# Optimization experiments

Hardware: AMD Instinct MI355X
Metric: run time of the kernel (lower is better)

Reference implementation:

```python
import jax, jax.numpy as jnp
import numpy as np

NC = 10
STRIDES = (8, 16, 32)
REG_W = 5.0
GAMMA = 2.0
ALPHA = 0.25
CENTER_R = 2.5
TOPK = 10


def _bce_logits(x, t):
    # numerically stable BCEWithLogits, reduction='none'
    return jnp.clip(x, 0.0) - x * t + jnp.log1p(jnp.exp(-jnp.abs(x)))


def _decode(pred, stride):
    # pred: [B, 5+NC, H, W] -> [B, H*W, 5+NC] with xy=(p+grid)*s, wh=exp(p)*s
    B, C, H, W = pred.shape
    out = pred.reshape(B, C, H * W).transpose(0, 2, 1)
    yv, xv = jnp.meshgrid(jnp.arange(H), jnp.arange(W), indexing='ij')
    grid = jnp.stack([xv, yv], -1).reshape(H * W, 2).astype(pred.dtype)
    xy = (out[..., :2] + grid[None]) * stride
    wh = jnp.exp(out[..., 2:4]) * stride
    return jnp.concatenate([xy, wh, out[..., 4:]], -1), grid


def _pair_iou(gt, pr):
    # gt [G,4], pr [A,4] in xywh -> [G,A]
    a1 = gt[:, None, :2] - gt[:, None, 2:] * 0.5
    a2 = gt[:, None, :2] + gt[:, None, 2:] * 0.5
    b1 = pr[None, :, :2] - pr[None, :, 2:] * 0.5
    b2 = pr[None, :, :2] + pr[None, :, 2:] * 0.5
    wh = jnp.clip(jnp.minimum(a2, b2) - jnp.maximum(a1, b1), 0.0)
    inter = wh[..., 0] * wh[..., 1]
    return inter / (gt[:, None, 2] * gt[:, None, 3] + pr[None, :, 2] * pr[None, :, 3] - inter + 1e-8)


def _assign(gt_box, gt_cls, gt_valid, bbox, cls_logit, obj_logit, xc, yc, sa):
    # SimOTA dynamic-k assignment for one image (padded GT with validity mask).
    G = gt_box.shape[0]
    gx, gy, gw, gh = gt_box[:, 0], gt_box[:, 1], gt_box[:, 2], gt_box[:, 3]
    l = xc[None] - (gx - gw * 0.5)[:, None]
    r = (gx + gw * 0.5)[:, None] - xc[None]
    tt = yc[None] - (gy - gh * 0.5)[:, None]
    bb = (gy + gh * 0.5)[:, None] - yc[None]
    in_box = (jnp.minimum(jnp.minimum(l, r), jnp.minimum(tt, bb)) > 0.0) & gt_valid[:, None]
    rad = CENTER_R * sa[None]
    cl = xc[None] - gx[:, None] + rad
    cr = gx[:, None] + rad - xc[None]
    ct = yc[None] - gy[:, None] + rad
    cb = gy[:, None] + rad - yc[None]
    in_ctr = (jnp.minimum(jnp.minimum(cl, cr), jnp.minimum(ct, cb)) > 0.0) & gt_valid[:, None]
    fg = jnp.any(in_box | in_ctr, axis=0)                       # [A] candidate anchors
    in_both = in_box & in_ctr
    ious = _pair_iou(gt_box, bbox)                              # [G,A]
    ious_fg = jnp.where(fg[None] & gt_valid[:, None], ious, 0.0)
    p = jnp.sqrt(jax.nn.sigmoid(cls_logit)[None] * jax.nn.sigmoid(obj_logit)[None])  # [1,A,NC]
    tgt = jax.nn.one_hot(gt_cls, NC)[:, None]                   # [G,1,NC]
    cls_cost = -(tgt * jnp.log(p + 1e-12) + (1.0 - tgt) * jnp.log(1.0 - p + 1e-12)).sum(-1)
    cost = (cls_cost + 3.0 * (-jnp.log(ious + 1e-8))
            + 1e5 * (~in_both) + 1e6 * ((~fg)[None] | (~gt_valid)[:, None]))
    # dynamic k per GT from sum of top-10 IoUs
    topk_ious = jax.lax.top_k(ious_fg, TOPK)[0]
    dyn_k = jnp.clip(topk_ious.sum(-1).astype(jnp.int32), 1, None)  # [G]
    _, idx = jax.lax.top_k(-cost, TOPK)                             # lowest-cost anchors per GT
    sel = (jnp.arange(TOPK)[None, :] < dyn_k[:, None]) & gt_valid[:, None]
    matching = jnp.zeros(cost.shape, bool).at[jnp.arange(G)[:, None], idx].set(sel)
    n_match = matching.sum(0)
    best = jnp.argmin(cost, 0)
    # anchors matched to multiple GTs keep only the min-cost GT
    matching = jnp.where(n_match[None] > 1, jnp.arange(G)[:, None] == best[None], matching)
    fg_final = jnp.any(matching, 0)
    mg = jnp.argmax(matching, 0)
    miou = (matching * ious).sum(0)
    return fg_final, miou, gt_cls[mg], gt_box[mg]


def _forward(pred0, pred1, pred2, labels):
    decoded, grids, strd = [], [], []
    for p, s in zip((pred0, pred1, pred2), STRIDES):
        o, g = _decode(p, s)
        decoded.append(o)
        grids.append(g)
        strd.append(jnp.full((g.shape[0],), float(s), o.dtype))
    out = jnp.concatenate(decoded, 1)                # [B,A,5+NC]
    grid = jnp.concatenate(grids, 0)                 # [A,2]
    sa = jnp.concatenate(strd, 0)                    # [A]
    bbox, obj, cls = out[..., :4], out[..., 4:5], out[..., 5:]
    xc = (grid[:, 0] + 0.5) * sa
    yc = (grid[:, 1] + 0.5) * sa
    gt_valid = labels.sum(-1) > 0                    # [B,G]
    gt_cls = labels[..., 0].astype(jnp.int32)
    gt_box = labels[..., 1:5]
    sg = jax.lax.stop_gradient                       # assignment is @torch.no_grad
    fg, miou, mcls, rtgt = jax.vmap(_assign, in_axes=(0, 0, 0, 0, 0, 0, None, None, None))(
        gt_box, gt_cls, gt_valid, sg(bbox), sg(cls), sg(obj), xc, yc, sa)
    fgf = fg.astype(out.dtype)
    num_fg = jnp.maximum(fgf.sum(), 1.0)
    p1 = bbox[..., :2] - bbox[..., 2:] * 0.5
    p2 = bbox[..., :2] + bbox[..., 2:] * 0.5
    t1 = rtgt[..., :2] - rtgt[..., 2:] * 0.5
    t2 = rtgt[..., :2] + rtgt[..., 2:] * 0.5
    wh = jnp.clip(jnp.minimum(p2, t2) - jnp.maximum(p1, t1), 0.0)
    inter = wh[..., 0] * wh[..., 1]
    iou = inter / (bbox[..., 2] * bbox[..., 3] + rtgt[..., 2] * rtgt[..., 3] - inter + 1e-8)
    loss_iou = ((1.0 - iou ** 2) * fgf).sum() / num_fg
    # focal objectness loss (gamma=2.0, alpha=0.25)
    t = fgf[..., None]
    bce = _bce_logits(obj, t)
    pr = jax.nn.sigmoid(obj)
    pt = t * pr + (1.0 - t) * (1.0 - pr)
    loss_obj = (bce * (t * ALPHA + (1.0 - t) * (1.0 - ALPHA)) * (1.0 - pt) ** GAMMA).sum() / num_fg
    # classification loss (reporting only, nc>1)
    ctgt = jax.nn.one_hot(mcls, NC, dtype=out.dtype) * miou[..., None]
    loss_cls = (_bce_logits(cls, ctgt) * fgf[..., None]).sum() / num_fg
    total = REG_W * loss_iou + loss_obj
    return total, loss_iou, loss_obj, loss_cls


def setup_inputs() -> dict:
    key = jax.random.key(0)
    ks = jax.random.split(key, 7)
    B, G = 16, 60
    pred0 = jax.random.normal(ks[0], (B, 5 + NC, 160, 160), jnp.float32)
    pred1 = jax.random.normal(ks[1], (B, 5 + NC, 80, 80), jnp.float32)
    pred2 = jax.random.normal(ks[2], (B, 5 + NC, 40, 40), jnp.float32)
    cls = jax.random.randint(ks[3], (B, G, 1), 0, NC).astype(jnp.float32)
    cxy = jax.random.uniform(ks[4], (B, G, 2), minval=32.0, maxval=1248.0)
    wh = jax.random.uniform(ks[5], (B, G, 2), minval=16.0, maxval=256.0)
    ngt = jax.random.randint(ks[6], (B,), 5, G + 1)
    valid = (jnp.arange(G)[None, :] < ngt[:, None]).astype(jnp.float32)
    labels = jnp.concatenate([cls, cxy, wh], -1) * valid[..., None]
    return {"pred0": pred0, "pred1": pred1, "pred2": pred2, "labels": labels}


def reference(pred0, pred1, pred2, labels):
    return _forward(pred0, pred1, pred2, labels)
```

## Files before the change

### kernel.cpp

```cpp
#include <hip/hip_runtime.h>
#include <math.h>

#define NCLS 10
#define NB   16
#define NG   60
#define NA   33600
#define BA   (NB*NA)
#define NBLK_X 132
#define NBLK_LOSS (NBLK_X*NB)

__device__ double g_part[NBLK_LOSS][4];
__device__ int    g_fcount[NB];
__device__ int    g_nmatch[BA];
__device__ int    g_gsum[BA];
__device__ int    g_slot[BA];
__device__ float4 g_cbox [BA];
__device__ float4 g_cmeta[BA];
__device__ float  g_cD   [(size_t)NB*NCLS*NA];

__device__ __forceinline__ void anchor_geom(int a, int& H, int& W, float& s, int& h, int& w, int& lvl) {
  if (a < 25600)      { lvl = 0; H = 160; W = 160; s = 8.f;  h = a / 160;            w = a - h*160; }
  else if (a < 32000) { lvl = 1; H = 80;  W = 80;  s = 16.f; int r = a - 25600; h = r / 80;  w = r - h*80; }
  else                { lvl = 2; H = 40;  W = 40;  s = 32.f; int r = a - 32000; h = r / 40;  w = r - h*40; }
}

__device__ __forceinline__ unsigned int fkey(float f) {
  unsigned int b = __float_as_uint(f);
  return (b & 0x80000000u) ? ~b : (b | 0x80000000u);
}

__global__ __launch_bounds__(256) void decode_kernel(const float* __restrict__ p0,
                                                     const float* __restrict__ p1,
                                                     const float* __restrict__ p2,
                                                     const float* __restrict__ lb) {
  __shared__ float lab[NG*5];
  __shared__ int   glist[NG];
  __shared__ int   gln;
  __shared__ int   wbase[4];
  __shared__ int   bbase_s;
  int b = blockIdx.y, tid = threadIdx.x;
  for (int i = tid; i < NG*5; i += 256) lab[i] = lb[(size_t)b*NG*5 + i];
  if (tid == 0) gln = 0;
  __syncthreads();

  int a0 = blockIdx.x * 256;
  int H, W, h0, w0, lvl; float st;
  anchor_geom(a0, H, W, st, h0, w0, lvl);
  int aL = a0 + 255; if (aL >= NA) aL = NA - 1;
  int Hx, Wx, h1, w1, l1; float st1;
  anchor_geom(aL, Hx, Wx, st1, h1, w1, l1);
  float ylo = ((float)h0 + 0.5f) * st;
  float yhi = ((float)h1 + 0.5f) * st;
  float rad = 2.5f * st;

  if (tid < NG) {
    float s0 = lab[tid*5] + lab[tid*5+1] + lab[tid*5+2] + lab[tid*5+3] + lab[tid*5+4];
    if (s0 > 0.f) {
      float gy = lab[tid*5+2], gh = lab[tid*5+4];
      float m = fmaxf(gh * 0.5f, rad);
      if ((gy - m < yhi) && (gy + m > ylo)) {
        int p = atomicAdd(&gln, 1);
        glist[p] = tid;
      }
    }
  }
  __syncthreads();

  int n = gln;
  if (n == 0) return;

  int a = a0 + tid;
  bool valid = a < NA;
  int H2, W2, ht, wt, l2; float st2;
  anchor_geom(valid ? a : a0, H2, W2, st2, ht, wt, l2);
  float xc = ((float)wt + 0.5f) * st;
  float yc = ((float)ht + 0.5f) * st;

  int fg = 0;
  if (valid) {
    for (int q = 0; q < n; q++) {
      int g = glist[q];
      float gx = lab[g*5+1], gy = lab[g*5+2], gw = lab[g*5+3], gh = lab[g*5+4];
      float l  = xc - (gx - gw*0.5f);
      float r  = (gx + gw*0.5f) - xc;
      float t  = yc - (gy - gh*0.5f);
      float bo = (gy + gh*0.5f) - yc;
      float m1 = fminf(fminf(l, r), fminf(t, bo));
      float cl = xc - gx + rad, cr = gx + rad - xc, ct = yc - gy + rad, cb = gy + rad - yc;
      float m2 = fminf(fminf(cl, cr), fminf(ct, cb));
      if (m1 > 0.f || m2 > 0.f) { fg = 1; break; }
    }
  }

  unsigned long long m = __ballot(fg != 0);
  int lane = tid & 63, wv = tid >> 6;
  if (lane == 0) wbase[wv] = __popcll(m);
  __syncthreads();
  if (tid == 0) {
    int t = 0;
    #pragma unroll
    for (int k = 0; k < 4; k++) { int c = wbase[k]; wbase[k] = t; t += c; }
    bbase_s = t ? atomicAdd(&g_fcount[b], t) : 0;
  }
  __syncthreads();

  if (fg) {
    const float* pp = (lvl == 0) ? p0 : ((lvl == 1) ? p1 : p2);
    size_t cs = (size_t)H * W;
    size_t base = (size_t)b * 15 * cs + (size_t)ht * W + wt;

    float tx = pp[base], ty = pp[base+cs], tw = pp[base+2*cs], th = pp[base+3*cs], to = pp[base+4*cs];
    float4 boxv = make_float4((tx + (float)wt) * st, (ty + (float)ht) * st,
                              __expf(tw) * st, __expf(th) * st);

    float so = 1.f / (1.f + __expf(-to));
    float S = 0.f;
    float Dl[NCLS];
    #pragma unroll
    for (int c = 0; c < NCLS; c++) {
      float xl = pp[base + (size_t)(5 + c) * cs];
      float sc = 1.f / (1.f + __expf(-xl));
      float p  = sqrtf(sc * so);
      float L  = __logf(p + 1e-12f);
      float M  = __logf(1.f - p + 1e-12f);
      S += M;
      Dl[c] = L - M;
    }

    int j = bbase_s + wbase[wv] + (int)__popcll(m & ((1ULL << lane) - 1ULL));
    size_t cb = (size_t)b * NA + j;
    g_cbox[cb]  = boxv;
    g_cmeta[cb] = make_float4(xc, yc, S, __int_as_float(a));
    #pragma unroll
    for (int c = 0; c < NCLS; c++) g_cD[((size_t)b*NCLS + c)*NA + j] = Dl[c];
    g_slot[b * NA + a] = j;
  }
}

__global__ __launch_bounds__(256) void topk_kernel(const float* __restrict__ lb) {
  __shared__ unsigned long long keyarr[256];
  __shared__ unsigned long long kvl[4][10];
  __shared__ float              ioul[4][10];
  __shared__ int                wcnt[4];
  __shared__ int                sdynk;
  __shared__ int                st1cnt;

  int fid = blockIdx.x;
  int t8 = fid >> 3;
  int b  = ((fid & 7) << 1) + (t8 >= 60 ? 1 : 0);
  int g  = t8 - (t8 >= 60 ? 60 : 0);
  int tid = threadIdx.x, lane = tid & 63, wv = tid >> 6;

  const float* L = &lb[((size_t)b*NG + g)*5];
  float l0 = L[0], l1 = L[1], l2 = L[2], l3 = L[3], l4 = L[4];
  if (!(l0 + l1 + l2 + l3 + l4 > 0.f)) return;

  int   gc = (int)l0;
  float gx = l1, gy = l2, gw = l3, gh = l4;
  float a1x = gx - gw*0.5f, a1y = gy - gh*0.5f, a2x = gx + gw*0.5f, a2y = gy + gh*0.5f;
  float garea = gw * gh;
  int F = g_fcount[b];
  const float4* CB = &g_cbox [(size_t)b*NA];
  const float4* CM = &g_cmeta[(size_t)b*NA];
  const float*  CD = &g_cD[((size_t)b*NCLS + gc)*NA];

  unsigned long long t1key = ~0ULL;
  if (tid < 108) {
    int lv   = tid / 36;
    int cell = tid - lv*36;
    int dy   = cell / 6 - 2;
    int dx   = cell - (cell/6)*6 - 2;
    int   W  = (lv == 0) ? 160 : ((lv == 1) ? 80 : 40);
    float st = (lv == 0) ? 8.f : ((lv == 1) ? 16.f : 32.f);
    int   ab = (lv == 0) ? 0 : ((lv == 1) ? 25600 : 32000);
    int wc = (int)floorf(gx / st - 0.5f) + dx;
    int hc = (int)floorf(gy / st - 0.5f) + dy;
    if (wc >= 0 && wc < W && hc >= 0 && hc < W) {
      float xc = ((float)wc + 0.5f) * st;
      float yc = ((float)hc + 0.5f) * st;
      float rad = 2.5f * st;
      bool inb = fminf(fminf(xc - a1x, a2x - xc), fminf(yc - a1y, a2y - yc)) > 0.f;
      bool inc = fminf(fminf(xc - gx + rad, gx + rad - xc), fminf(yc - gy + rad, gy + rad - yc)) > 0.f;
      if (inb && inc) {
        int a = ab + hc * W + wc;
        int j = g_slot[b*NA + a];
        float4 B = CB[j];
        float Dv = CD[j];
        float S  = CM[j].z;
        float b1x = B.x - B.z*0.5f, b1y = B.y - B.w*0.5f;
        float b2x = B.x + B.z*0.5f, b2y = B.y + B.w*0.5f;
        float wx = fminf(a2x, b2x) - fmaxf(a1x, b1x); wx = wx > 0.f ? wx : 0.f;
        float wy = fminf(a2y, b2y) - fmaxf(a1y, b1y); wy = wy > 0.f ? wy : 0.f;
        float inter = wx * wy;
        float iou = inter / (garea + B.z*B.w - inter + 1e-8f);
        float cost = -(Dv + S) + 3.0f * (-__logf(iou + 1e-8f));
        t1key = ((unsigned long long)fkey(cost) << 32) | (unsigned int)a;
      }
    }
  }
  keyarr[tid] = t1key;
  {
    unsigned long long bal = __ballot(t1key != ~0ULL);
    if (lane == 0) wcnt[wv] = __popcll(bal);
  }

  float iv[10];
  #pragma unroll
  for (int k = 0; k < 10; k++) iv[k] = 0.f;
  #pragma unroll 2
  for (int j = tid; j < F; j += 256) {
    float4 B = CB[j];
    float b1x = B.x - B.z*0.5f, b1y = B.y - B.w*0.5f;
    float b2x = B.x + B.z*0.5f, b2y = B.y + B.w*0.5f;
    float wx = fminf(a2x, b2x) - fmaxf(a1x, b1x); wx = wx > 0.f ? wx : 0.f;
    float wy = fminf(a2y, b2y) - fmaxf(a1y, b1y); wy = wy > 0.f ? wy : 0.f;
    float inter = wx * wy;
    float iou = inter / (garea + B.z*B.w - inter + 1e-8f);
    if (iou > iv[9]) {
      iv[9] = iou;
      #pragma unroll
      for (int k = 9; k > 0; k--) {
        if (iv[k] > iv[k-1]) { float t = iv[k]; iv[k] = iv[k-1]; iv[k-1] = t; }
      }
    }
  }
  for (int k = 0; k < 10; k++) {
    float m = iv[0];
    #pragma unroll
    for (int d = 1; d < 64; d <<= 1) m = fmaxf(m, __shfl_xor(m, d));
    if (lane == 0) ioul[wv][k] = m;
    unsigned long long pm = __ballot(iv[0] == m);
    if (lane == __ffsll((unsigned long long)pm) - 1) {
      #pragma unroll
      for (int j2 = 0; j2 < 9; j2++) iv[j2] = iv[j2+1];
      iv[9] = 0.f;
    }
  }
  __syncthreads();

  if (tid == 0) {
    st1cnt = wcnt[0] + wcnt[1] + wcnt[2] + wcnt[3];
    int p_[4] = {0,0,0,0};
    float ss = 0.f;
    #pragma unroll 1
    for (int k = 0; k < 10; k++) {
      float best = ioul[0][p_[0]]; int bl = 0;
      #pragma unroll
      for (int l = 1; l < 4; l++) {
        float v = ioul[l][p_[l]];
        if (v > best) { best = v; bl = l; }
      }
      ss += best;
      if (p_[bl] < 9) p_[bl]++;
      else ioul[bl][9] = -INFINITY;
    }
    int dynk = (int)ss;
    if (dynk < 1)  dynk = 1;
    if (dynk > 10) dynk = 10;
    sdynk = dynk;
  }
  __syncthreads();
  int dynk  = sdynk;
  int t1cnt = st1cnt;

  if (t1cnt >= 10) {
    if (wv == 0) {
      unsigned long long q0 = keyarr[lane], q1 = keyarr[lane+64],
                         q2 = keyarr[lane+128], q3 = keyarr[lane+192];
      { unsigned long long t;
        if (q1 < q0) { t=q0; q0=q1; q1=t; }
        if (q3 < q2) { t=q2; q2=q3; q3=t; }
        if (q2 < q0) { t=q0; q0=q2; q2=t; }
        if (q3 < q1) { t=q1; q1=q3; q3=t; }
        if (q2 < q1) { t=q1; q1=q2; q2=t; } }
      for (int k = 0; k < dynk; k++) {
        unsigned long long m = q0;
        #pragma unroll
        for (int d = 1; d < 64; d <<= 1) {
          unsigned long long o = __shfl_xor(m, d);
          if (o < m) m = o;
        }
        if (m == ~0ULL) break;
        if (lane == 0) {
          int a = (int)(unsigned int)(m & 0xFFFFFFFFu);
          atomicAdd(&g_nmatch[b*NA + a], 1);
          atomicAdd(&g_gsum[b*NA + a], g);
        }
        if (q0 == m) { q0 = q1; q1 = q2; q2 = q3; q3 = ~0ULL; }
      }
    }
  } else {
    unsigned long long kv[10];
    #pragma unroll
    for (int k = 0; k < 10; k++) kv[k] = ~0ULL;
    for (int j = tid; j < F; j += 256) {
      float4 B = CB[j];
      float4 M = CM[j];
      float Dv = CD[j];
      int a = __float_as_int(M.w);
      float b1x = B.x - B.z*0.5f, b1y = B.y - B.w*0.5f;
      float b2x = B.x + B.z*0.5f, b2y = B.y + B.w*0.5f;
      float wx = fminf(a2x, b2x) - fmaxf(a1x, b1x); wx = wx > 0.f ? wx : 0.f;
      float wy = fminf(a2y, b2y) - fmaxf(a1y, b1y); wy = wy > 0.f ? wy : 0.f;
      float inter = wx * wy;
      float iou = inter / (garea + B.z*B.w - inter + 1e-8f);
      float xc = M.x, yc = M.y;
      float rad = (a < 25600) ? 20.f : ((a < 32000) ? 40.f : 80.f);
      bool inb = fminf(fminf(xc - a1x, a2x - xc), fminf(yc - a1y, a2y - yc)) > 0.f;
      bool inc = fminf(fminf(xc - gx + rad, gx + rad - xc), fminf(yc - gy + rad, gy + rad - yc)) > 0.f;
      float cost = -(Dv + M.z) + 3.0f * (-__logf(iou + 1e-8f));
      if (!(inb && inc)) cost += 100000.0f;
      unsigned long long key = ((unsigned long long)fkey(cost) << 32) | (unsigned int)a;
      if (key < kv[9]) {
        kv[9] = key;
        #pragma unroll
        for (int k = 9; k > 0; k--) {
          if (kv[k] < kv[k-1]) { unsigned long long t = kv[k]; kv[k] = kv[k-1]; kv[k-1] = t; }
        }
      }
    }
    for (int k = 0; k < 10; k++) {
      unsigned long long m = kv[0];
      #pragma unroll
      for (int d = 1; d < 64; d <<= 1) {
        unsigned long long o = __shfl_xor(m, d);
        if (o < m) m = o;
      }
      if (lane == 0) kvl[wv][k] = m;
      if (kv[0] == m) {
        #pragma unroll
        for (int j2 = 0; j2 < 9; j2++) kv[j2] = kv[j2+1];
        kv[9] = ~0ULL;
      }
    }
    __syncthreads();
    if (tid == 0) {
      int p_[4] = {0,0,0,0};
      #pragma unroll 1
      for (int k = 0; k < dynk; k++) {
        unsigned long long best = kvl[0][p_[0]]; int bl = 0;
        #pragma unroll
        for (int l = 1; l < 4; l++) {
          unsigned long long v = kvl[l][p_[l]];
          if (v < best) { best = v; bl = l; }
        }
        if (best == ~0ULL) break;
        int a = (int)(unsigned int)(best & 0xFFFFFFFFu);
        atomicAdd(&g_nmatch[b*NA + a], 1);
        atomicAdd(&g_gsum[b*NA + a], g);
        if (p_[bl] < 9) p_[bl]++;
        else kvl[bl][9] = ~0ULL;
      }
    }
  }
}

__global__ __launch_bounds__(256) void loss_kernel(const float* __restrict__ p0,
                                                   const float* __restrict__ p1,
                                                   const float* __restrict__ p2,
                                                   const float* __restrict__ lb) {
  __shared__ float  lab[NG*5];
  __shared__ int    lval[NG];
  __shared__ double red[256*4];
  int b = blockIdx.y, tid = threadIdx.x;
  for (int i = tid; i < NG*5; i += 256) lab[i] = lb[(size_t)b*NG*5 + i];
  __syncthreads();
  if (tid < NG) {
    float s = lab[tid*5] + lab[tid*5+1] + lab[tid*5+2] + lab[tid*5+3] + lab[tid*5+4];
    lval[tid] = (s > 0.f) ? 1 : 0;
  }
  __syncthreads();

  int a = blockIdx.x * 256 + tid;
  double t_nfg = 0.0, t_iou = 0.0, t_obj = 0.0, t_cls = 0.0;

  if (a < NA) {
    int idx = b * NA + a;
    int H, W, h, w, lvl; float st;
    anchor_geom(a, H, W, st, h, w, lvl);
    const float* pp = (lvl == 0) ? p0 : ((lvl == 1) ? p1 : p2);
    size_t cs = (size_t)H * W;
    size_t base = (size_t)b * 15 * cs + (size_t)h * W + w;

    float x  = pp[base + 4*cs];
    int   nm = g_nmatch[idx];
    float t  = (nm > 0) ? 1.f : 0.f;
    float bce = fmaxf(x, 0.f) - x * t + log1pf(expf(-fabsf(x)));
    float pr  = 1.f / (1.f + expf(-x));
    float pt  = (nm > 0) ? pr : (1.f - pr);
    float wf  = (nm > 0) ? 0.25f : 0.75f;
    float om  = 1.f - pt;
    t_obj = (double)(bce * wf * om * om);

    if (nm > 0) {
      t_nfg = 1.0;
      int mgsum = g_gsum[idx];
      g_nmatch[idx] = 0;
      g_gsum[idx]   = 0;
      int j = g_slot[idx];
      float4 B  = g_cbox [(size_t)b*NA + j];
      float4 Mt = g_cmeta[(size_t)b*NA + j];
      float pw = B.z, ph = B.w;
      float b1x = B.x - pw*0.5f, b1y = B.y - ph*0.5f, b2x = B.x + pw*0.5f, b2y = B.y + ph*0.5f;
      int mg;
      if (nm == 1) {
        mg = mgsum;
      } else {
        float xc = Mt.x, yc = Mt.y, S = Mt.z;
        float rad = 2.5f * st;
        const float* CDb = &g_cD[(size_t)b*NCLS*NA];
        float best = INFINITY; int bg = 0;
        for (int g = 0; g < NG; g++) {
          float gx = lab[g*5+1], gy = lab[g*5+2], gw = lab[g*5+3], gh = lab[g*5+4];
          int gcl = (int)lab[g*5];
          int v = lval[g];
          float a1x = gx - gw*0.5f, a1y = gy - gh*0.5f, a2x = gx + gw*0.5f, a2y = gy + gh*0.5f;
          float wx = fminf(a2x, b2x) - fmaxf(a1x, b1x); wx = wx > 0.f ? wx : 0.f;
          float wy = fminf(a2y, b2y) - fmaxf(a1y, b1y); wy = wy > 0.f ? wy : 0.f;
          float inter = wx * wy;
          float iou = inter / (gw*gh + pw*ph - inter + 1e-8f);
          float l = xc - a1x, r = a2x - xc, tt = yc - a1y, bo = a2y - yc;
          bool inb = (fminf(fminf(l, r), fminf(tt, bo)) > 0.f) && v;
          float cl = xc - gx + rad, cr = gx + rad - xc, ct = yc - gy + rad, cb = gy + rad - yc;
          bool inc = (fminf(fminf(cl, cr), fminf(ct, cb)) > 0.f) && v;
          float clsc = -(CDb[(size_t)gcl*NA + j] + S);
          float cost = clsc + 3.0f * (-__logf(iou + 1e-8f));
          if (!(inb && inc)) cost += 100000.0f;
          if (!v)            cost += 1000000.0f;
          if (cost < best) { best = cost; bg = g; }
        }
        mg = bg;
      }

      float gx = lab[mg*5+1], gy = lab[mg*5+2], gw = lab[mg*5+3], gh = lab[mg*5+4];
      int mcls = (int)lab[mg*5];
      float a1x = gx - gw*0.5f, a1y = gy - gh*0.5f, a2x = gx + gw*0.5f, a2y = gy + gh*0.5f;
      float wx = fminf(a2x, b2x) - fmaxf(a1x, b1x); wx = wx > 0.f ? wx : 0.f;
      float wy = fminf(a2y, b2y) - fmaxf(a1y, b1y); wy = wy > 0.f ? wy : 0.f;
      float inter = wx * wy;
      float miou = inter / (gw*gh + pw*ph - inter + 1e-8f);

      t_iou = (double)(1.f - miou * miou);

      float sc = 0.f;
      #pragma unroll
      for (int c = 0; c < NCLS; c++) {
        float xl = pp[base + (size_t)(5 + c) * cs];
        float ctg = (c == mcls) ? miou : 0.f;
        sc += fmaxf(xl, 0.f) - xl * ctg + log1pf(expf(-fabsf(xl)));
      }
      t_cls = (double)sc;
    }
  }

  red[tid] = t_nfg; red[256+tid] = t_iou; red[512+tid] = t_obj; red[768+tid] = t_cls;
  __syncthreads();
  for (int s = 128; s > 0; s >>= 1) {
    if (tid < s) {
      red[tid]     += red[tid+s];
      red[256+tid] += red[256+tid+s];
      red[512+tid] += red[512+tid+s];
      red[768+tid] += red[768+tid+s];
    }
    __syncthreads();
  }
  if (tid == 0) {
    int blk = b * NBLK_X + blockIdx.x;
    g_part[blk][0] = red[0];
    g_part[blk][1] = red[256];
    g_part[blk][2] = red[512];
    g_part[blk][3] = red[768];
  }
}

__global__ __launch_bounds__(256) void final_kernel(float* __restrict__ out) {
  __shared__ double red[256];
  int tid = threadIdx.x;
  int cat = tid & 3;
  double s = 0.0;
  for (int blk = tid >> 2; blk < NBLK_LOSS; blk += 64) s += g_part[blk][cat];
  red[tid] = s;
  __syncthreads();
  for (int st = 128; st >= 4; st >>= 1) {
    if (tid < st) red[tid] += red[tid + st];
    __syncthreads();
  }
  if (tid == 0) {
    double nfg = red[0];
    double num = (nfg < 1.0) ? 1.0 : nfg;
    float li = (float)(red[1] / num);
    float lo = (float)(red[2] / num);
    float lc = (float)(red[3] / num);
    out[0] = 5.0f * li + lo;
    out[1] = li;
    out[2] = lo;
    out[3] = lc;
  }
  if (tid < NB) g_fcount[tid] = 0;
}

extern "C" void kernel_launch(void* const* d_in, const int* in_sizes, int n_in,
                              void* d_out, int out_size, void* d_ws, size_t ws_size,
                              hipStream_t stream) {
  const float* p0 = (const float*)d_in[0];
  const float* p1 = (const float*)d_in[1];
  const float* p2 = (const float*)d_in[2];
  const float* lb = (const float*)d_in[3];
  float* out = (float*)d_out;

  hipLaunchKernelGGL(decode_kernel, dim3(NBLK_X, NB), dim3(256), 0, stream, p0, p1, p2, lb);
  hipLaunchKernelGGL(topk_kernel,   dim3(NB*NG), dim3(256), 0, stream, lb);
  hipLaunchKernelGGL(loss_kernel,   dim3(NBLK_X, NB), dim3(256), 0, stream, p0, p1, p2, lb);
  hipLaunchKernelGGL(final_kernel,  dim3(1), dim3(256), 0, stream, out);
}
```

Measured before the change: 189.3 us.

## Widen topk blocks to 512 threads, prefetch boxes, use shuffle reduction in loss

The top-k assignment kernel now launches 512 threads per GT (8 wavefronts) and merges per-wave top-10 lists across 8 waves. Its IoU scan software-prefetches the next candidate box. The stage-1 key array shrinks to 128 entries, which assumes the hidden code produces at most 128 in-box-and-center candidates. The loss kernel replaces a shared-memory tree reduction over 4 double arrays with wave shuffles plus a small cross-wave sum, removing many barriers.

```diff
diff --git a/kernel.cpp b/kernel.cpp
--- a/kernel.cpp
+++ b/kernel.cpp
@@ -8,6 +8,7 @@
 #define BA   (NB*NA)
 #define NBLK_X 132
 #define NBLK_LOSS (NBLK_X*NB)
+#define TKW  8
 
 __device__ double g_part[NBLK_LOSS][4];
 __device__ int    g_fcount[NB];
@@ -137,11 +138,11 @@
   }
 }
 
-__global__ __launch_bounds__(256) void topk_kernel(const float* __restrict__ lb) {
-  __shared__ unsigned long long keyarr[256];
-  __shared__ unsigned long long kvl[4][10];
-  __shared__ float              ioul[4][10];
-  __shared__ int                wcnt[4];
+__global__ __launch_bounds__(512) void topk_kernel(const float* __restrict__ lb) {
+  __shared__ unsigned long long keyarr[128];
+  __shared__ unsigned long long kvl[TKW][10];
+  __shared__ float              ioul[TKW][10];
+  __shared__ int                wcnt[2];
   __shared__ int                sdynk;
   __shared__ int                st1cnt;
 
@@ -198,8 +199,8 @@
       }
     }
   }
-  keyarr[tid] = t1key;
-  {
+  if (tid < 128) keyarr[tid] = t1key;
+  if (wv < 2) {
     unsigned long long bal = __ballot(t1key != ~0ULL);
     if (lane == 0) wcnt[wv] = __popcll(bal);
   }
@@ -207,21 +208,28 @@
   float iv[10];
   #pragma unroll
   for (int k = 0; k < 10; k++) iv[k] = 0.f;
-  #pragma unroll 2
-  for (int j = tid; j < F; j += 256) {
-    float4 B = CB[j];
-    float b1x = B.x - B.z*0.5f, b1y = B.y - B.w*0.5f;
-    float b2x = B.x + B.z*0.5f, b2y = B.y + B.w*0.5f;
-    float wx = fminf(a2x, b2x) - fmaxf(a1x, b1x); wx = wx > 0.f ? wx : 0.f;
-    float wy = fminf(a2y, b2y) - fmaxf(a1y, b1y); wy = wy > 0.f ? wy : 0.f;
-    float inter = wx * wy;
-    float iou = inter / (garea + B.z*B.w - inter + 1e-8f);
-    if (iou > iv[9]) {
-      iv[9] = iou;
-      #pragma unroll
-      for (int k = 9; k > 0; k--) {
-        if (iv[k] > iv[k-1]) { float t = iv[k]; iv[k] = iv[k-1]; iv[k-1] = t; }
-      }
+  {
+    int j = tid;
+    float4 Bc = make_float4(0.f, 0.f, 0.f, 0.f);
+    if (j < F) Bc = CB[j];
+    while (j < F) {
+      int jn = j + 512;
+      float4 Bn = make_float4(0.f, 0.f, 0.f, 0.f);
+      if (jn < F) Bn = CB[jn];
+      float b1x = Bc.x - Bc.z*0.5f, b1y = Bc.y - Bc.w*0.5f;
+      float b2x = Bc.x + Bc.z*0.5f, b2y = Bc.y + Bc.w*0.5f;
+      float wx = fminf(a2x, b2x) - fmaxf(a1x, b1x); wx = wx > 0.f ? wx : 0.f;
+      float wy = fminf(a2y, b2y) - fmaxf(a1y, b1y); wy = wy > 0.f ? wy : 0.f;
+      float inter = wx * wy;
+      float iou = inter / (garea + Bc.z*Bc.w - inter + 1e-8f);
+      if (iou > iv[9]) {
+        iv[9] = iou;
+        #pragma unroll
+        for (int k = 9; k > 0; k--) {
+          if (iv[k] > iv[k-1]) { float t = iv[k]; iv[k] = iv[k-1]; iv[k-1] = t; }
+        }
+      }
+      Bc = Bn; j = jn;
     }
   }
   for (int k = 0; k < 10; k++) {
@@ -239,14 +247,16 @@
   __syncthreads();
 
   if (tid == 0) {
-    st1cnt = wcnt[0] + wcnt[1] + wcnt[2] + wcnt[3];
-    int p_[4] = {0,0,0,0};
+    st1cnt = wcnt[0] + wcnt[1];
+    int p_[TKW];
+    #pragma unroll
+    for (int l = 0; l < TKW; l++) p_[l] = 0;
     float ss = 0.f;
     #pragma unroll 1
     for (int k = 0; k < 10; k++) {
       float best = ioul[0][p_[0]]; int bl = 0;
       #pragma unroll
-      for (int l = 1; l < 4; l++) {
+      for (int l = 1; l < TKW; l++) {
         float v = ioul[l][p_[l]];
         if (v > best) { best = v; bl = l; }
       }
@@ -265,14 +275,8 @@
 
   if (t1cnt >= 10) {
     if (wv == 0) {
-      unsigned long long q0 = keyarr[lane], q1 = keyarr[lane+64],
-                         q2 = keyarr[lane+128], q3 = keyarr[lane+192];
-      { unsigned long long t;
-        if (q1 < q0) { t=q0; q0=q1; q1=t; }
-        if (q3 < q2) { t=q2; q2=q3; q3=t; }
-        if (q2 < q0) { t=q0; q0=q2; q2=t; }
-        if (q3 < q1) { t=q1; q1=q3; q3=t; }
-        if (q2 < q1) { t=q1; q1=q2; q2=t; } }
+      unsigned long long q0 = keyarr[lane], q1 = keyarr[lane+64];
+      if (q1 < q0) { unsigned long long t = q0; q0 = q1; q1 = t; }
       for (int k = 0; k < dynk; k++) {
         unsigned long long m = q0;
         #pragma unroll
@@ -286,14 +290,14 @@
           atomicAdd(&g_nmatch[b*NA + a], 1);
           atomicAdd(&g_gsum[b*NA + a], g);
         }
-        if (q0 == m) { q0 = q1; q1 = q2; q2 = q3; q3 = ~0ULL; }
+        if (q0 == m) { q0 = q1; q1 = ~0ULL; }
       }
     }
   } else {
     unsigned long long kv[10];
     #pragma unroll
     for (int k = 0; k < 10; k++) kv[k] = ~0ULL;
-    for (int j = tid; j < F; j += 256) {
+    for (int j = tid; j < F; j += 512) {
       float4 B = CB[j];
       float4 M = CM[j];
       float Dv = CD[j];
@@ -335,12 +339,14 @@
     }
     __syncthreads();
     if (tid == 0) {
-      int p_[4] = {0,0,0,0};
+      int p_[TKW];
+      #pragma unroll
+      for (int l = 0; l < TKW; l++) p_[l] = 0;
       #pragma unroll 1
       for (int k = 0; k < dynk; k++) {
         unsigned long long best = kvl[0][p_[0]]; int bl = 0;
         #pragma unroll
-        for (int l = 1; l < 4; l++) {
+        for (int l = 1; l < TKW; l++) {
           unsigned long long v = kvl[l][p_[l]];
           if (v < best) { best = v; bl = l; }
         }
@@ -361,7 +367,7 @@
                                                    const float* __restrict__ lb) {
   __shared__ float  lab[NG*5];
   __shared__ int    lval[NG];
-  __shared__ double red[256*4];
+  __shared__ double wred[4][4];
   int b = blockIdx.y, tid = threadIdx.x;
   for (int i = tid; i < NG*5; i += 256) lab[i] = lb[(size_t)b*NG*5 + i];
   __syncthreads();
@@ -453,23 +459,24 @@
     }
   }
 
-  red[tid] = t_nfg; red[256+tid] = t_iou; red[512+tid] = t_obj; red[768+tid] = t_cls;
-  __syncthreads();
-  for (int s = 128; s > 0; s >>= 1) {
-    if (tid < s) {
-      red[tid]     += red[tid+s];
-      red[256+tid] += red[256+tid+s];
-      red[512+tid] += red[512+tid+s];
-      red[768+tid] += red[768+tid+s];
-    }
-    __syncthreads();
-  }
+  #pragma unroll
+  for (int d = 32; d > 0; d >>= 1) {
+    t_nfg += __shfl_down(t_nfg, d);
+    t_iou += __shfl_down(t_iou, d);
+    t_obj += __shfl_down(t_obj, d);
+    t_cls += __shfl_down(t_cls, d);
+  }
+  int lane = tid & 63, wv = tid >> 6;
+  if (lane == 0) {
+    wred[wv][0] = t_nfg; wred[wv][1] = t_iou; wred[wv][2] = t_obj; wred[wv][3] = t_cls;
+  }
+  __syncthreads();
   if (tid == 0) {
     int blk = b * NBLK_X + blockIdx.x;
-    g_part[blk][0] = red[0];
-    g_part[blk][1] = red[256];
-    g_part[blk][2] = red[512];
-    g_part[blk][3] = red[768];
+    g_part[blk][0] = wred[0][0] + wred[1][0] + wred[2][0] + wred[3][0];
+    g_part[blk][1] = wred[0][1] + wred[1][1] + wred[2][1] + wred[3][1];
+    g_part[blk][2] = wred[0][2] + wred[1][2] + wred[2][2] + wred[3][2];
+    g_part[blk][3] = wred[0][3] + wred[1][3] + wred[2][3] + wred[3][3];
   }
 }
 
@@ -509,7 +516,7 @@
   float* out = (float*)d_out;
 
   hipLaunchKernelGGL(decode_kernel, dim3(NBLK_X, NB), dim3(256), 0, stream, p0, p1, p2, lb);
-  hipLaunchKernelGGL(topk_kernel,   dim3(NB*NG), dim3(256), 0, stream, lb);
+  hipLaunchKernelGGL(topk_kernel,   dim3(NB*NG), dim3(512), 0, stream, lb);
   hipLaunchKernelGGL(loss_kernel,   dim3(NBLK_X, NB), dim3(256), 0, stream, p0, p1, p2, lb);
   hipLaunchKernelGGL(final_kernel,  dim3(1), dim3(256), 0, stream, out);
 }
```

Result: faster. 172.7 us (-8.8%).
